# Kernel tuning notes

Measured on AMD Instinct MI355X. Metric: run time of the kernel, lower is better.

The kernel has to match this reference:

```python
import jax, jax.numpy as jnp
import numpy as np

NH = 8        # num_heads
HD = 6        # head_dim
DIM = NH * HD # 48
KS = 3        # kernel_size
NT = KS ** 3  # 27 neighborhood tokens
SCALE = HD ** -0.5


def setup_inputs() -> dict:
    key = jax.random.key(0)
    k1, k2, k3 = jax.random.split(key, 3)
    B, H, W, T = 1, 40, 40, 40
    q = jax.random.normal(k1, (B, H, W, T, DIM), jnp.float32)
    k = jax.random.normal(k2, (B, H, W, T, DIM), jnp.float32)
    # learned relative position bias (torch init is zeros; use small noise so it matters)
    rpb = jax.random.normal(k3, (NH, KS, KS, KS), jnp.float32) * 0.02
    return {"q": q, "k": k, "rpb": rpb}


def _neighborhood_attention(q, k, rpb):
    B, H, W, T, C = q.shape
    # pad keys by win_size=1 on each spatial side (zero pad, as in nnf.pad)
    kp = jnp.pad(k, ((0, 0), (1, 1), (1, 1), (1, 1), (0, 0)))
    # gather the 27 shifted views -> [B,H,W,T,27,C] (equivalent of unfold+permute)
    win = jnp.stack(
        [kp[:, i:i + H, j:j + W, l:l + T, :]
         for i in range(KS) for j in range(KS) for l in range(KS)],
        axis=4,
    )
    qh = q.reshape(B, H, W, T, NH, HD) * SCALE          # [B,H,W,T,nh,hd]
    kh = win.reshape(B, H, W, T, NT, NH, HD)            # [B,H,W,T,27,nh,hd]
    attn = jnp.einsum('bxyzhd,bxyzkhd->bxyzhk', qh, kh)
    attn = attn + rpb.reshape(NH, NT)[None, None, None, None]  # rel-pos bias
    attn = jax.nn.softmax(attn, axis=-1)                # [B,H,W,T,nh,27]
    # value = constant integer offsets of the 3x3x3 window (makeV)
    r = jnp.arange(-(KS // 2), KS // 2 + 1, dtype=q.dtype)
    offs = jnp.stack(jnp.meshgrid(r, r, r, indexing='ij'), axis=-1).reshape(NT, 3)
    out = jnp.einsum('bxyzhk,ko->bxyzho', attn, offs)   # [B,H,W,T,nh,3]
    return out.reshape(B, H, W, T, NH * 3).transpose(0, 4, 1, 2, 3)


def reference(q, k, rpb):
    return _neighborhood_attention(q, k, rpb)
```

## Files before the change

### kernel.cpp

```cpp
#include <hip/hip_runtime.h>


#define GS   40
#define NVOX (GS*GS*GS)
#define VST  36

typedef __fp16 half2_t __attribute__((ext_vector_type(2)));
typedef float  f2      __attribute__((ext_vector_type(2)));

__device__ __forceinline__ float fdot2(half2_t a, half2_t b, float c) {
    return __builtin_amdgcn_fdot2(a, b, c, false);
}
__device__ __forceinline__ half2_t h2(unsigned int u) {
    return __builtin_bit_cast(half2_t, u);
}
__device__ __forceinline__ unsigned int pk(float a, float b) {
    return __builtin_bit_cast(unsigned int, __builtin_amdgcn_cvt_pkrtz(a, b));
}

__global__ __launch_bounds__(256) void natt_kernel(
    const float* __restrict__ q, const float* __restrict__ kk,
    const float* __restrict__ rpb, float* __restrict__ out)
{
    __shared__ __align__(16) unsigned int sk[224 * VST];
    __shared__ float srpb[4 * 72];
    __shared__ int   vtab[224];

    int t = threadIdx.x;
    int b = blockIdx.x;
    int w = (b & 7) * 125 + (b >> 3);
    int bz = w % 10, by = (w / 10) % 10, bx = w / 100;
    int x0 = bx * 4, y0 = by * 4, z0 = bz * 4;

    int hp = t & 3;
    int v  = t >> 2;
    int vz = v & 3, vy = (v >> 2) & 3, vx = v >> 4;
    int gvox = (x0 + vx) * 1600 + (y0 + vy) * 40 + (z0 + vz);
    const float4* qp = (const float4*)q + (size_t)gvox * 12 + hp * 3;
    float4 qa = qp[0], qb = qp[1], qc = qp[2];

    if (t < 224) {
        int vvc = t < 216 ? t : 215;
        int xi = vvc / 36, r36 = vvc - xi * 36;
        int yi = r36 / 6,  zi  = r36 - yi * 6;
        int gx = x0 + xi - 1, gy = y0 + yi - 1, gz = z0 + zi - 1;
        bool val = (((unsigned)gx < GS) & ((unsigned)gy < GS) &
                    ((unsigned)gz < GS)) && (t < 216);
        int cx = min(max(gx, 0), GS - 1);
        int cy = min(max(gy, 0), GS - 1);
        int cz = min(max(gz, 0), GS - 1);
        vtab[t] = ((cx * 1600 + cy * 40 + cz) * 12) | (val ? (1 << 30) : 0);
    }
    if (t < 216) {
        int h = t / 27, n = t - h * 27;
        int i = n / 9, r9 = n - i * 9;
        int j = r9 / 3, l = r9 - j * 3;
        srpb[(h >> 1) * 72 + ((i * 3 + j) * 4 + l) * 2 + (h & 1)] =
            rpb[t] * 1.4426950408889634f;
    }
    __syncthreads();

    {
        const float4* kk4 = (const float4*)kk;
        int sub = t & 7;
        int hpc = sub >> 1, pt = sub & 1;
        int soffA = hpc * 3 + pt * 2;
        int soffB = soffA + (pt ? 0 : 1);
        unsigned int* dstb = sk + (t >> 3) * VST + hpc * 8 + pt * 4;
        const int* vtp = vtab + (t >> 3);
        #pragma unroll
        for (int it = 0; it < 7; ++it) {
            int rec = vtp[it * 32];
            unsigned m = (unsigned)(((int)(rec << 1)) >> 31);
            int base = rec & 0x3FFFFFFF;
            float4 fA = kk4[base + soffA];
            float4 fB = kk4[base + soffB];
            uint4 u;
            u.x = pk(fA.x, fA.y) & m; u.y = pk(fA.z, fA.w) & m;
            u.z = pk(fB.x, fB.y) & m; u.w = pk(fB.z, fB.w) & m;
            *(uint4*)(dstb + it * 32 * VST) = u;
        }
    }

    const float QS = 0.4082482904638631f * 1.4426950408889634f;
    half2_t qh0 = __builtin_amdgcn_cvt_pkrtz(qa.x*QS, qa.y*QS);
    half2_t qh1 = __builtin_amdgcn_cvt_pkrtz(qa.z*QS, qa.w*QS);
    half2_t qh2 = __builtin_amdgcn_cvt_pkrtz(qb.x*QS, qb.y*QS);
    half2_t qh3 = __builtin_amdgcn_cvt_pkrtz(qb.z*QS, qb.w*QS);
    half2_t qh4 = __builtin_amdgcn_cvt_pkrtz(qc.x*QS, qc.y*QS);
    half2_t qh5 = __builtin_amdgcn_cvt_pkrtz(qc.z*QS, qc.w*QS);

    __syncthreads();

    const unsigned int* kbp = sk + (vx * 36 + vy * 6 + vz) * VST + hp * 8;
    const float* rbp = srpb + hp * 72;

    f2 den = {0,0}, ozc = {0,0};
    f2 xp = {0,0}, xm = {0,0}, yp = {0,0}, ym = {0,0};

    #pragma unroll
    for (int i = 0; i < 3; ++i)
    #pragma unroll
    for (int j = 0; j < 3; ++j) {
        const unsigned int* cb = kbp + (i * 36 + j * 6) * VST;
        float4 rp01 = *(const float4*)(rbp + (i * 3 + j) * 8);
        f2     rp2v = *(const f2*)(rbp + (i * 3 + j) * 8 + 4);
        f2 ev[3];
        #pragma unroll
        for (int l = 0; l < 3; ++l) {
            uint4 a = *(const uint4*)(cb + l * VST);
            uint2 c = *(const uint2*)(cb + l * VST + 4);
            float rx = (l == 0) ? rp01.x : (l == 1) ? rp01.z : rp2v.x;
            float ry = (l == 0) ? rp01.y : (l == 1) ? rp01.w : rp2v.y;
            float d0 = fdot2(qh0, h2(a.x),
                       fdot2(qh1, h2(a.y),
                       fdot2(qh2, h2(a.z), rx)));
            float d1 = fdot2(qh3, h2(a.w),
                       fdot2(qh4, h2(c.x),
                       fdot2(qh5, h2(c.y), ry)));
            ev[l].x = __builtin_amdgcn_exp2f(d0);
            ev[l].y = __builtin_amdgcn_exp2f(d1);
        }
        f2 A = ev[0] + ev[1] + ev[2];
        den += A;
        ozc += ev[2] - ev[0];
        if (i == 0)      xm += A;
        else if (i == 2) xp += A;
        if (j == 0)      ym += A;
        else if (j == 2) yp += A;
    }

    f2 oxv = xp - xm, oyv = yp - ym;
    float inv0 = __builtin_amdgcn_rcpf(den.x);
    float inv1 = __builtin_amdgcn_rcpf(den.y);

    float* op = out + (size_t)(hp * 6) * NVOX + gvox;
    op[0*NVOX] = oxv.x * inv0;
    op[1*NVOX] = oyv.x * inv0;
    op[2*NVOX] = ozc.x * inv0;
    op[3*NVOX] = oxv.y * inv1;
    op[4*NVOX] = oyv.y * inv1;
    op[5*NVOX] = ozc.y * inv1;
}

extern "C" void kernel_launch(void* const* d_in, const int* in_sizes, int n_in,
                              void* d_out, int out_size, void* d_ws, size_t ws_size,
                              hipStream_t stream) {
    const float* q   = (const float*)d_in[0];
    const float* k   = (const float*)d_in[1];
    const float* rpb = (const float*)d_in[2];
    float* out = (float*)d_out;

    natt_kernel<<<1000, 256, 0, stream>>>(q, k, rpb, out);
}
```

Before: 14.45 us.

## Enlarge tiles to 8x4x4 voxels with 512-thread blocks and per-voxel halo loads

```diff
diff --git a/kernel.cpp b/kernel.cpp
--- a/kernel.cpp
+++ b/kernel.cpp
@@ -18,19 +18,19 @@
     return __builtin_bit_cast(unsigned int, __builtin_amdgcn_cvt_pkrtz(a, b));
 }
 
-__global__ __launch_bounds__(256) void natt_kernel(
+__global__ __launch_bounds__(512, 4) void natt_kernel(
     const float* __restrict__ q, const float* __restrict__ kk,
     const float* __restrict__ rpb, float* __restrict__ out)
 {
-    __shared__ __align__(16) unsigned int sk[224 * VST];
+    __shared__ __align__(16) unsigned int sk[360 * VST];
     __shared__ float srpb[4 * 72];
-    __shared__ int   vtab[224];
 
     int t = threadIdx.x;
     int b = blockIdx.x;
-    int w = (b & 7) * 125 + (b >> 3);
+    int xcd = b & 7, off = b >> 3;
+    int w = (xcd < 4 ? xcd * 63 : 252 + (xcd - 4) * 62) + off;
     int bz = w % 10, by = (w / 10) % 10, bx = w / 100;
-    int x0 = bx * 4, y0 = by * 4, z0 = bz * 4;
+    int x0 = bx * 8, y0 = by * 4, z0 = bz * 4;
 
     int hp = t & 3;
     int v  = t >> 2;
@@ -39,18 +39,6 @@
     const float4* qp = (const float4*)q + (size_t)gvox * 12 + hp * 3;
     float4 qa = qp[0], qb = qp[1], qc = qp[2];
 
-    if (t < 224) {
-        int vvc = t < 216 ? t : 215;
-        int xi = vvc / 36, r36 = vvc - xi * 36;
-        int yi = r36 / 6,  zi  = r36 - yi * 6;
-        int gx = x0 + xi - 1, gy = y0 + yi - 1, gz = z0 + zi - 1;
-        bool val = (((unsigned)gx < GS) & ((unsigned)gy < GS) &
-                    ((unsigned)gz < GS)) && (t < 216);
-        int cx = min(max(gx, 0), GS - 1);
-        int cy = min(max(gy, 0), GS - 1);
-        int cz = min(max(gz, 0), GS - 1);
-        vtab[t] = ((cx * 1600 + cy * 40 + cz) * 12) | (val ? (1 << 30) : 0);
-    }
     if (t < 216) {
         int h = t / 27, n = t - h * 27;
         int i = n / 9, r9 = n - i * 9;
@@ -58,27 +46,31 @@
         srpb[(h >> 1) * 72 + ((i * 3 + j) * 4 + l) * 2 + (h & 1)] =
             rpb[t] * 1.4426950408889634f;
     }
-    __syncthreads();
 
-    {
-        const float4* kk4 = (const float4*)kk;
-        int sub = t & 7;
-        int hpc = sub >> 1, pt = sub & 1;
-        int soffA = hpc * 3 + pt * 2;
-        int soffB = soffA + (pt ? 0 : 1);
-        unsigned int* dstb = sk + (t >> 3) * VST + hpc * 8 + pt * 4;
-        const int* vtp = vtab + (t >> 3);
+    if (t < 360) {
+        int hx = t / 36, r36 = t - hx * 36;
+        int hy = r36 / 6, hz = r36 - hy * 6;
+        int gx = x0 + hx - 1, gy = y0 + hy - 1, gz = z0 + hz - 1;
+        unsigned m = (((unsigned)gx < GS) & ((unsigned)gy < GS) &
+                      ((unsigned)gz < GS)) ? 0xffffffffu : 0u;
+        int cx = min(max(gx, 0), GS - 1);
+        int cy = min(max(gy, 0), GS - 1);
+        int cz = min(max(gz, 0), GS - 1);
+        const float4* src = (const float4*)kk +
+                            (size_t)(cx * 1600 + cy * 40 + cz) * 12;
+        unsigned int* dst = sk + t * VST;
         #pragma unroll
-        for (int it = 0; it < 7; ++it) {
-            int rec = vtp[it * 32];
-            unsigned m = (unsigned)(((int)(rec << 1)) >> 31);
-            int base = rec & 0x3FFFFFFF;
-            float4 fA = kk4[base + soffA];
-            float4 fB = kk4[base + soffB];
-            uint4 u;
-            u.x = pk(fA.x, fA.y) & m; u.y = pk(fA.z, fA.w) & m;
-            u.z = pk(fB.x, fB.y) & m; u.w = pk(fB.z, fB.w) & m;
-            *(uint4*)(dstb + it * 32 * VST) = u;
+        for (int hpc = 0; hpc < 4; ++hpc) {
+            float4 f0 = src[hpc * 3 + 0];
+            float4 f1 = src[hpc * 3 + 1];
+            float4 fv = src[hpc * 3 + 2];
+            uint4 u4v;
+            u4v.x = pk(f0.x, f0.y) & m; u4v.y = pk(f0.z, f0.w) & m;
+            u4v.z = pk(f1.x, f1.y) & m; u4v.w = pk(f1.z, f1.w) & m;
+            uint2 u2v;
+            u2v.x = pk(fv.x, fv.y) & m; u2v.y = pk(fv.z, fv.w) & m;
+            *(uint4*)(dst + hpc * 8)     = u4v;
+            *(uint2*)(dst + hpc * 8 + 4) = u2v;
         }
     }
 
@@ -151,5 +143,5 @@
     const float* rpb = (const float*)d_in[2];
     float* out = (float*)d_out;
 
-    natt_kernel<<<1000, 256, 0, stream>>>(q, k, rpb, out);
+    natt_kernel<<<500, 512, 0, stream>>>(q, k, rpb, out);
 }
```

New measurement: 13.98 us. -3.3%, faster.
